# Kernel optimization log

Hardware: AMD Instinct MI355X
Metric: run time of the kernel (lower is better)

The kernel has to match this reference:

```python
import jax, jax.numpy as jnp
import numpy as np

B, T, H, W, C = 4, 16, 56, 56, 256
NH = 8
CS = (2, 7, 7)   # cuboid_size
SS = (1, 3, 3)   # shift_size


def _reorder(x):
    # (B,T,H,W,C) -> (B, num_cuboids, cuboid_volume, C), strategy 'lll'
    b = x.shape[0]
    bt, bh, bw = CS
    x = x.reshape(b, T // bt, bt, H // bh, bh, W // bw, bw, C)
    x = x.transpose(0, 1, 3, 5, 2, 4, 6, 7)
    return x.reshape(b, (T // bt) * (H // bh) * (W // bw), bt * bh * bw, C)


def _reorder_rev(x):
    b = x.shape[0]
    bt, bh, bw = CS
    x = x.reshape(b, T // bt, H // bh, W // bw, bt, bh, bw, C)
    x = x.transpose(0, 1, 4, 2, 5, 3, 6, 7)
    return x.reshape(b, T, H, W, C)


def _attn_mask():
    # shift-window mask, computed statically with numpy (no padding needed:
    # T,H,W divide CS exactly, so data_mask is all-ones)
    m = np.zeros((T, H, W))
    cnt = 0
    for t in (slice(-CS[0]), slice(-CS[0], -SS[0]), slice(-SS[0], None)):
        for h in (slice(-CS[1]), slice(-CS[1], -SS[1]), slice(-SS[1], None)):
            for w in (slice(-CS[2]), slice(-CS[2], -SS[2]), slice(-SS[2], None)):
                m[t, h, w] = cnt
                cnt += 1
    bt, bh, bw = CS
    m = m.reshape(T // bt, bt, H // bh, bh, W // bw, bw)
    m = m.transpose(0, 2, 4, 1, 3, 5).reshape(-1, bt * bh * bw)
    return jnp.asarray(m[:, None, :] == m[:, :, None])  # (num_cuboids, vol, vol)


def setup_inputs() -> dict:
    key = jax.random.key(0)
    k1, k2, k3 = jax.random.split(key, 3)
    return {
        "x": jax.random.normal(k1, (B, T, H, W, C), dtype=jnp.float32),
        "gamma": jnp.ones((C,), jnp.float32),
        "beta": jnp.zeros((C,), jnp.float32),
        "w_qkv": jax.random.normal(k2, (3 * C, C), jnp.float32) * 0.02,
        "w_proj": jax.random.normal(k3, (C, C), jnp.float32) * 0.02,
        "b_proj": jnp.zeros((C,), jnp.float32),
    }


def reference(x, gamma, beta, w_qkv, w_proj, b_proj):
    hd = C // NH
    scale = hd ** -0.5
    # pre-norm (LayerNorm, eps=1e-5, biased variance as in torch)
    mu = x.mean(-1, keepdims=True)
    var = x.var(-1, keepdims=True)
    xn = (x - mu) * jax.lax.rsqrt(var + 1e-5) * gamma + beta
    # shift then cuboid reorder
    xs = jnp.roll(xn, shift=(-SS[0], -SS[1], -SS[2]), axis=(1, 2, 3))
    r = _reorder(xs)                       # (B, nc, vol, C)
    nc, vol = r.shape[1], r.shape[2]
    qkv = jnp.einsum('bnvc,dc->bnvd', r, w_qkv).reshape(B, nc, vol, 3, NH, hd)
    qkv = qkv.transpose(3, 0, 4, 1, 2, 5)  # (3, B, NH, nc, vol, hd)
    q, k, v = qkv[0], qkv[1], qkv[2]
    mask = _attn_mask()                    # (nc, vol, vol) bool
    score = jnp.einsum('bhnic,bhnjc->bhnij', q * scale, k)
    score = jnp.where(mask, score, jnp.float32(-1e18))
    attn = jax.nn.softmax(score, axis=-1) * mask  # masked_softmax
    out = jnp.einsum('bhnij,bhnjc->bhnic', attn, v)
    out = out.transpose(0, 2, 3, 1, 4).reshape(B, nc, vol, C)
    out = jnp.einsum('bnvc,dc->bnvd', out, w_proj) + b_proj  # final proj
    y = _reorder_rev(out)
    y = jnp.roll(y, shift=(SS[0], SS[1], SS[2]), axis=(1, 2, 3))
    return y
```

## Files before the change

kernel.cpp:

```cpp
#include <hip/hip_runtime.h>
#include <hip/hip_bf16.h>

#define NC_  512
#define VOL_ 98

typedef __attribute__((ext_vector_type(8))) short bf16x8;
typedef __attribute__((ext_vector_type(4))) float f32x4;
typedef __attribute__((ext_vector_type(16))) float f32x16;
typedef unsigned int u32;
typedef unsigned short u16;

#define MFMA16(a,b,c) __builtin_amdgcn_mfma_f32_16x16x32_bf16((a),(b),(c),0,0,0)
#define MFMA32(a,b,c) __builtin_amdgcn_mfma_f32_32x32x16_bf16((a),(b),(c),0,0,0)

#define SWZ(r)   ((unsigned)(((r) & 7) << 4))
#define SWZ5(r)  ((unsigned)(((r) & 31) << 4))
#define SWZV(d)  ((unsigned)(((d) & 15) << 4))

__device__ __forceinline__ u16 f2bf(float f) {
    u32 u = __float_as_uint(f);
    u32 r = (u + 0x7fffu + ((u >> 16) & 1u)) >> 16;
    return (u16)r;
}
__device__ __forceinline__ u32 cvt_pk(float lo, float hi) {
    u32 r;
    asm("v_cvt_pk_bf16_f32 %0, %1, %2" : "=v"(r) : "v"(lo), "v"(hi));
    return r;
}

__global__ void k_conv(const float* __restrict__ wqkv, const float* __restrict__ wproj,
                       u16* __restrict__ o)
{
    int i = blockIdx.x * 256 + threadIdx.x;
    if (i < 196608) {
        float v = wqkv[i];
        if (i < 65536) v *= 0.17677669529663687f;
        o[i] = f2bf(v);
    } else if (i < 262144) {
        o[i] = f2bf(wproj[i - 196608]);
    }
}

__global__ __launch_bounds__(512, 4)
void k_attn(const float* __restrict__ x, const float* __restrict__ gamma,
            const float* __restrict__ beta, const u16* __restrict__ wbf,
            u16* __restrict__ ao)
{
    __shared__ __align__(16) u16 rn[VOL_ * 256];
    __shared__ __align__(16) u16 Qs[112 * 32];
    __shared__ __align__(16) u16 Ks[112 * 32];
    __shared__ __align__(16) u16 Vt[32 * 128];
    __shared__ u32 rowbase[112];
    __shared__ unsigned char labs[128];

    const int rawb = blockIdx.x;
    const int bid = ((rawb & 7) << 8) | (rawb >> 3);
    const int b  = bid >> 9, n = bid & 511;
    const int ti = n >> 6, hi = (n >> 3) & 7, wi = n & 7;
    const int tid = threadIdx.x;
    const int lane = tid & 63, wv = tid >> 6;
    const int c15 = lane & 15, g  = lane >> 4;
    const int c31 = lane & 31, g2 = lane >> 5;

    if (tid < 128) {
        int i = tid;
        int vt = (i >= 49) ? 1 : 0;
        int r  = i - vt * 49;
        int vh = r / 7, vw = r - vh * 7;
        int t = ti * 2 + vt, h = hi * 7 + vh, w = wi * 7 + vw;
        if (i < 112) {
            int ts = (t + 1) & 15;
            int hs = h + 3; if (hs >= 56) hs -= 56;
            int ws2 = w + 3; if (ws2 >= 56) ws2 -= 56;
            rowbase[i] = (i < VOL_) ? (u32)((((b * 16 + ts) * 56 + hs) * 56 + ws2) * 256) : 0u;
        }
        if (i < VOL_) {
            int tr = (t < 14) ? 0 : ((t < 15) ? 1 : 2);
            int hr = (h < 49) ? 0 : ((h < 53) ? 1 : 2);
            int wr = (w < 49) ? 0 : ((w < 53) ? 1 : 2);
            labs[i] = (unsigned char)(tr * 9 + hr * 3 + wr);
        } else {
            labs[i] = (unsigned char)255;
        }
    }
    if (tid < 256) {
        int d = tid >> 3, kp = 112 + (tid & 7) * 2;
        unsigned a = (unsigned)(d * 256 + kp * 2) ^ SWZV(d);
        *(u32*)((char*)Vt + a) = 0u;
    }
    __syncthreads();

    const float4 gm = *(const float4*)(gamma + lane * 4);
    const float4 be = *(const float4*)(beta  + lane * 4);
    for (int i = wv; i < VOL_; i += 8) {
        const float* xp = x + (size_t)rowbase[i] + lane * 4;
        float4 xv = *(const float4*)xp;
        float s  = xv.x + xv.y + xv.z + xv.w;
        float s2 = xv.x * xv.x + xv.y * xv.y + xv.z * xv.z + xv.w * xv.w;
        #pragma unroll
        for (int o = 1; o < 64; o <<= 1) { s += __shfl_xor(s, o); s2 += __shfl_xor(s2, o); }
        float mu  = s  * (1.0f / 256.0f);
        float var = s2 * (1.0f / 256.0f) - mu * mu;
        float rs  = rsqrtf(var + 1e-5f);
        unsigned a = ((unsigned)(i * 512 + lane * 8)) ^ SWZ5(i);
        uint2 pk2;
        pk2.x = cvt_pk((xv.x - mu) * rs * gm.x + be.x, (xv.y - mu) * rs * gm.y + be.y);
        pk2.y = cvt_pk((xv.z - mu) * rs * gm.z + be.z, (xv.w - mu) * rs * gm.w + be.w);
        *(uint2*)((char*)rn + a) = pk2;
    }

    u32 lab4[7];
    #pragma unroll
    for (int c = 0; c < 7; ++c) lab4[c] = *(const u32*)&labs[c * 16 + g * 4];

    for (int hh = 0; hh < 8; ++hh) {
        __syncthreads();

        for (int u = wv; u < 12; u += 8) {
            int proj = u >> 2, mt = u & 3;
            int arow = mt * 32 + c31; if (arow > 111) arow = 111;
            const u16* wb = wbf + (size_t)(proj * 256 + hh * 32 + c31) * 256 + g2 * 8;
            f32x16 acc = {0,0,0,0,0,0,0,0,0,0,0,0,0,0,0,0};
            #pragma unroll
            for (int half = 0; half < 2; ++half) {
                bf16x8 Bf[8];
                #pragma unroll
                for (int kk = 0; kk < 8; ++kk)
                    Bf[kk] = *(const bf16x8*)(wb + (half * 8 + kk) * 16);
                #pragma unroll
                for (int kk = 0; kk < 8; ++kk) {
                    unsigned a = (unsigned)(arow * 512 + (half * 8 + kk) * 32 + g2 * 16) ^ SWZ5(arow);
                    bf16x8 A = *(const bf16x8*)((const char*)rn + a);
                    acc = MFMA32(A, Bf[kk], acc);
                }
            }
            if (proj == 2) {
                #pragma unroll
                for (int r = 0; r < 16; r += 2) {
                    int kpos = mt * 32 + (r & 3) + 8 * (r >> 2) + 4 * g2;
                    float v0 = (kpos < VOL_)     ? acc[r]     : 0.f;
                    float v1 = (kpos + 1 < VOL_) ? acc[r + 1] : 0.f;
                    unsigned a = (unsigned)(c31 * 256 + kpos * 2) ^ SWZV(c31);
                    *(u32*)((char*)Vt + a) = cvt_pk(v0, v1);
                }
            } else {
                char* dst = (char*)((proj == 0) ? Qs : Ks);
                #pragma unroll
                for (int r = 0; r < 16; ++r) {
                    int grow = mt * 32 + (r & 3) + 8 * (r >> 2) + 4 * g2;
                    if (grow < 112) {
                        unsigned a = (unsigned)(grow * 64 + c31 * 2) ^ SWZ(grow);
                        *(u16*)(dst + a) = f2bf(acc[r]);
                    }
                }
            }
        }
        __syncthreads();

        for (int mt = wv; mt < 7; mt += 8) {
            int qrow = mt * 16 + c15;
            int labr = labs[qrow];
            u32 labr4 = (u32)labr * 0x01010101u;
            unsigned qa = (unsigned)(qrow * 64 + g * 16) ^ SWZ(qrow);
            bf16x8 qB = *(const bf16x8*)((const char*)Qs + qa);

            f32x4 s[7];
            #pragma unroll
            for (int c = 0; c < 7; ++c) {
                int krow = c * 16 + c15;
                unsigned ka = (unsigned)(krow * 64 + g * 16) ^ SWZ(krow);
                bf16x8 kA = *(const bf16x8*)((const char*)Ks + ka);
                f32x4 z = {0.f, 0.f, 0.f, 0.f};
                s[c] = MFMA16(kA, qB, z);
            }
            float mx = -1e30f;
            #pragma unroll
            for (int c = 0; c < 7; ++c) {
                u32 xo = lab4[c] ^ labr4;
                #pragma unroll
                for (int i = 0; i < 4; ++i) {
                    bool ok = ((xo >> (8 * i)) & 255u) == 0u;
                    mx = fmaxf(mx, ok ? s[c][i] : -1e30f);
                }
            }
            mx = fmaxf(mx, __shfl_xor(mx, 16));
            mx = fmaxf(mx, __shfl_xor(mx, 32));
            float lsum = 0.f;
            #pragma unroll
            for (int c = 0; c < 7; ++c) {
                u32 xo = lab4[c] ^ labr4;
                #pragma unroll
                for (int i = 0; i < 4; ++i) {
                    bool ok = ((xo >> (8 * i)) & 255u) == 0u;
                    float e = ok ? __expf(s[c][i] - mx) : 0.f;
                    s[c][i] = e;
                    lsum += e;
                }
            }
            lsum += __shfl_xor(lsum, 16);
            lsum += __shfl_xor(lsum, 32);
            float inv = 1.0f / lsum;
            u32 pk[8][2];
            #pragma unroll
            for (int c = 0; c < 7; ++c) {
                pk[c][0] = cvt_pk(s[c][0] * inv, s[c][1] * inv);
                pk[c][1] = cvt_pk(s[c][2] * inv, s[c][3] * inv);
            }
            pk[7][0] = 0u; pk[7][1] = 0u;

            f32x4 O0 = {0.f, 0.f, 0.f, 0.f}, O1 = {0.f, 0.f, 0.f, 0.f};
            const int src0 = c15 + 32 * (g & 1);
            const bool csel = (g >> 1) != 0;
            #pragma unroll
            for (int f = 0; f < 4; ++f) {
                union { bf16x8 v; u32 w[4]; } pa;
                #pragma unroll
                for (int w = 0; w < 4; ++w) {
                    int src = src0 + 16 * (w >> 1);
                    u32 r0 = (u32)__shfl((int)pk[2 * f][w & 1], src);
                    u32 r1 = (u32)__shfl((int)pk[2 * f + 1][w & 1], src);
                    pa.w[w] = csel ? r1 : r0;
                }
                unsigned av0 = (unsigned)(c15 * 256 + f * 64 + g * 16) ^ SWZV(c15);
                unsigned av1 = (unsigned)((16 + c15) * 256 + f * 64 + g * 16) ^ SWZV(16 + c15);
                bf16x8 vB0 = *(const bf16x8*)((const char*)Vt + av0);
                bf16x8 vB1 = *(const bf16x8*)((const char*)Vt + av1);
                O0 = MFMA16(pa.v, vB0, O0);
                O1 = MFMA16(pa.v, vB1, O1);
            }
            #pragma unroll
            for (int i = 0; i < 4; ++i) {
                int grow = mt * 16 + g * 4 + i;
                if (grow < VOL_) {
                    size_t base = ((size_t)bid * VOL_ + grow) * 256 + hh * 32;
                    ao[base + c15]      = f2bf(O0[i]);
                    ao[base + 16 + c15] = f2bf(O1[i]);
                }
            }
        }
    }
}

__global__ __launch_bounds__(512, 4)
void k_proj(const u16* __restrict__ ao, const u16* __restrict__ wpbf,
            const float* __restrict__ bp, float* __restrict__ y)
{
    __shared__ __align__(16) u16 tile[VOL_ * 256];
    __shared__ u32 rowbase[112];
    const int rawb = blockIdx.x;
    const int bid = ((rawb & 7) << 8) | (rawb >> 3);
    const int b  = bid >> 9, n = bid & 511;
    const int ti = n >> 6, hi = (n >> 3) & 7, wi = n & 7;
    const int tid = threadIdx.x;
    const int c31 = (tid & 63) & 31, g2 = (tid & 63) >> 5;
    const int wv = tid >> 6;

    if (tid < 112) {
        int i = tid;
        int vt = (i >= 49) ? 1 : 0;
        int r  = i - vt * 49;
        int vh = r / 7, vw = r - vh * 7;
        int t = ti * 2 + vt, h = hi * 7 + vh, w = wi * 7 + vw;
        int ts = (t + 1) & 15;
        int hs = h + 3; if (hs >= 56) hs -= 56;
        int ws2 = w + 3; if (ws2 >= 56) ws2 -= 56;
        rowbase[i] = (i < VOL_) ? (u32)((((b * 16 + ts) * 56 + hs) * 56 + ws2) * 256) : 0u;
    }
    const uint4* src = (const uint4*)(ao + (size_t)bid * (VOL_ * 256));
    for (int cidx = tid; cidx < (VOL_ * 256) / 8; cidx += 512) {
        uint4 v = src[cidx];
        int row = cidx >> 5, blk = cidx & 31;
        unsigned a = (unsigned)((row << 9) + (blk << 4)) ^ SWZ5(row);
        *(uint4*)((char*)tile + a) = v;
    }
    __syncthreads();

    for (int u = wv; u < 32; u += 8) {
        int nt = u >> 2, mt = u & 3;
        int arow = mt * 32 + c31; if (arow > 97) arow = 97;
        const u16* wb = wpbf + (size_t)(nt * 32 + c31) * 256 + g2 * 8;
        f32x16 acc = {0,0,0,0,0,0,0,0,0,0,0,0,0,0,0,0};
        #pragma unroll
        for (int half = 0; half < 2; ++half) {
            bf16x8 Bf[8];
            #pragma unroll
            for (int kk = 0; kk < 8; ++kk)
                Bf[kk] = *(const bf16x8*)(wb + (half * 8 + kk) * 16);
            #pragma unroll
            for (int kk = 0; kk < 8; ++kk) {
                unsigned a = (unsigned)(arow * 512 + (half * 8 + kk) * 32 + g2 * 16) ^ SWZ5(arow);
                bf16x8 A = *(const bf16x8*)((const char*)tile + a);
                acc = MFMA32(A, Bf[kk], acc);
            }
        }
        float bias = bp[nt * 32 + c31];
        #pragma unroll
        for (int r = 0; r < 16; ++r) {
            int row = (r & 3) + 8 * (r >> 2) + 4 * g2 + mt * 32;
            if (row < VOL_) {
                y[(size_t)rowbase[row] + nt * 32 + c31] = acc[r] + bias;
            }
        }
    }
}

extern "C" void kernel_launch(void* const* d_in, const int* in_sizes, int n_in,
                              void* d_out, int out_size, void* d_ws, size_t ws_size,
                              hipStream_t stream) {
    const float* x     = (const float*)d_in[0];
    const float* gamma = (const float*)d_in[1];
    const float* beta  = (const float*)d_in[2];
    const float* wqkv  = (const float*)d_in[3];
    const float* wproj = (const float*)d_in[4];
    const float* bproj = (const float*)d_in[5];
    float* y = (float*)d_out;

    u16* wbf  = (u16*)d_ws;
    u16* wpbf = wbf + 196608;
    u16* ao   = wbf + 262144;

    k_conv<<<dim3(1024), dim3(256), 0, stream>>>(wqkv, wproj, wbf);
    k_attn<<<dim3(4 * NC_), dim3(512), 0, stream>>>(x, gamma, beta, wbf, ao);
    k_proj<<<dim3(4 * NC_), dim3(512), 0, stream>>>(ao, wpbf, bproj, y);
}
```

Baseline: 613.1 us.

## Move Q projection into per-wave attention tiles to balance K/V projection work

The K and V projections (8 units) now map one-to-one onto the 8 waves, replacing the 12-unit round-robin where 4 waves did double work. Each attention wave computes its own 16-row Q tile with 16x16 MFMAs just before the score computation, which removes the Q projection from the shared stage. This trades a less imbalanced barrier-separated phase for some redundant A-operand LDS reads and an extra lgkmcnt wait. It also guards the softmax against a zero row sum.

```diff
diff --git a/kernel.cpp b/kernel.cpp
--- a/kernel.cpp
+++ b/kernel.cpp
@@ -90,23 +90,25 @@
     }
     __syncthreads();
 
-    const float4 gm = *(const float4*)(gamma + lane * 4);
-    const float4 be = *(const float4*)(beta  + lane * 4);
-    for (int i = wv; i < VOL_; i += 8) {
-        const float* xp = x + (size_t)rowbase[i] + lane * 4;
-        float4 xv = *(const float4*)xp;
-        float s  = xv.x + xv.y + xv.z + xv.w;
-        float s2 = xv.x * xv.x + xv.y * xv.y + xv.z * xv.z + xv.w * xv.w;
-        #pragma unroll
-        for (int o = 1; o < 64; o <<= 1) { s += __shfl_xor(s, o); s2 += __shfl_xor(s2, o); }
-        float mu  = s  * (1.0f / 256.0f);
-        float var = s2 * (1.0f / 256.0f) - mu * mu;
-        float rs  = rsqrtf(var + 1e-5f);
-        unsigned a = ((unsigned)(i * 512 + lane * 8)) ^ SWZ5(i);
-        uint2 pk2;
-        pk2.x = cvt_pk((xv.x - mu) * rs * gm.x + be.x, (xv.y - mu) * rs * gm.y + be.y);
-        pk2.y = cvt_pk((xv.z - mu) * rs * gm.z + be.z, (xv.w - mu) * rs * gm.w + be.w);
-        *(uint2*)((char*)rn + a) = pk2;
+    {
+        const float4 gm = *(const float4*)(gamma + lane * 4);
+        const float4 be = *(const float4*)(beta  + lane * 4);
+        for (int i = wv; i < VOL_; i += 8) {
+            const float* xp = x + (size_t)rowbase[i] + lane * 4;
+            float4 xv = *(const float4*)xp;
+            float s  = xv.x + xv.y + xv.z + xv.w;
+            float s2 = xv.x * xv.x + xv.y * xv.y + xv.z * xv.z + xv.w * xv.w;
+            #pragma unroll
+            for (int o = 1; o < 64; o <<= 1) { s += __shfl_xor(s, o); s2 += __shfl_xor(s2, o); }
+            float mu  = s  * (1.0f / 256.0f);
+            float var = s2 * (1.0f / 256.0f) - mu * mu;
+            float rs  = rsqrtf(var + 1e-5f);
+            unsigned a = ((unsigned)(i * 512 + lane * 8)) ^ SWZ5(i);
+            uint2 pk2;
+            pk2.x = cvt_pk((xv.x - mu) * rs * gm.x + be.x, (xv.y - mu) * rs * gm.y + be.y);
+            pk2.y = cvt_pk((xv.z - mu) * rs * gm.z + be.z, (xv.w - mu) * rs * gm.w + be.w);
+            *(uint2*)((char*)rn + a) = pk2;
+        }
     }
 
     u32 lab4[7];
@@ -116,8 +118,9 @@
     for (int hh = 0; hh < 8; ++hh) {
         __syncthreads();
 
-        for (int u = wv; u < 12; u += 8) {
-            int proj = u >> 2, mt = u & 3;
+        {
+            const int proj = (wv >> 2) + 1;
+            const int mt = wv & 3;
             int arow = mt * 32 + c31; if (arow > 111) arow = 111;
             const u16* wb = wbf + (size_t)(proj * 256 + hh * 32 + c31) * 256 + g2 * 8;
             f32x16 acc = {0,0,0,0,0,0,0,0,0,0,0,0,0,0,0,0};
@@ -144,20 +147,45 @@
                     *(u32*)((char*)Vt + a) = cvt_pk(v0, v1);
                 }
             } else {
-                char* dst = (char*)((proj == 0) ? Qs : Ks);
                 #pragma unroll
                 for (int r = 0; r < 16; ++r) {
                     int grow = mt * 32 + (r & 3) + 8 * (r >> 2) + 4 * g2;
                     if (grow < 112) {
                         unsigned a = (unsigned)(grow * 64 + c31 * 2) ^ SWZ(grow);
-                        *(u16*)(dst + a) = f2bf(acc[r]);
+                        *(u16*)((char*)Ks + a) = f2bf(acc[r]);
                     }
                 }
             }
         }
         __syncthreads();
 
-        for (int mt = wv; mt < 7; mt += 8) {
+        if (wv < 7) {
+            const int mt = wv;
+            {
+                int jr = mt * 16 + c15; if (jr > 97) jr = 97;
+                #pragma unroll
+                for (int ct = 0; ct < 2; ++ct) {
+                    const u16* wq = wbf + (size_t)(hh * 32 + ct * 16 + c15) * 256 + g * 8;
+                    f32x4 acc = {0.f, 0.f, 0.f, 0.f};
+                    #pragma unroll
+                    for (int kk = 0; kk < 8; ++kk) {
+                        unsigned a = (unsigned)(jr * 512 + kk * 64 + g * 16) ^ SWZ5(jr);
+                        bf16x8 A = *(const bf16x8*)((const char*)rn + a);
+                        bf16x8 B = *(const bf16x8*)(wq + kk * 32);
+                        acc = MFMA16(A, B, acc);
+                    }
+                    int colb = ct * 16 + c15;
+                    #pragma unroll
+                    for (int i = 0; i < 4; ++i) {
+                        int grow = mt * 16 + g * 4 + i;
+                        unsigned a = (unsigned)(grow * 64 + colb * 2) ^ SWZ(grow);
+                        *(u16*)((char*)Qs + a) = f2bf(acc[i]);
+                    }
+                }
+                asm volatile("s_waitcnt lgkmcnt(0)" ::: "memory");
+                __builtin_amdgcn_sched_barrier(0);
+            }
+
             int qrow = mt * 16 + c15;
             int labr = labs[qrow];
             u32 labr4 = (u32)labr * 0x01010101u;
@@ -199,7 +227,7 @@
             }
             lsum += __shfl_xor(lsum, 16);
             lsum += __shfl_xor(lsum, 32);
-            float inv = 1.0f / lsum;
+            float inv = (lsum > 0.f) ? (1.0f / lsum) : 0.f;
             u32 pk[8][2];
             #pragma unroll
             for (int c = 0; c < 7; ++c) {
@@ -208,7 +236,7 @@
             }
             pk[7][0] = 0u; pk[7][1] = 0u;
 
-            f32x4 O0 = {0.f, 0.f, 0.f, 0.f}, O1 = {0.f, 0.f, 0.f, 0.f};
+            f32x4 O0 = {0.f,0.f,0.f,0.f}, O1 = {0.f,0.f,0.f,0.f};
             const int src0 = c15 + 32 * (g & 1);
             const bool csel = (g >> 1) != 0;
             #pragma unroll
```

New measurement: 703.4 us. +14.7%, slower.

## Overlap next-head Q projection with attention via double-buffered Q tile

Applied to the files above, without the earlier changes.

Double-buffers the Q shared-memory tile. While waves 0-6 run attention for head hh, wave 7 computes the Q projection for head hh+1, so each later head only projects K and V (8 units across the 8 waves) inside the synchronized phase. The 32x32 GEMM unit is moved into a helper that splits accumulation across two independent MFMA chains to shorten the dependency chain. This costs extra LDS for the second Q buffer, and the lone Q-producing wave may become the critical path each iteration.

```diff
diff --git a/kernel.cpp b/kernel.cpp
--- a/kernel.cpp
+++ b/kernel.cpp
@@ -26,6 +26,27 @@
     u32 r;
     asm("v_cvt_pk_bf16_f32 %0, %1, %2" : "=v"(r) : "v"(lo), "v"(hi));
     return r;
+}
+
+__device__ __forceinline__ f32x16 unit32(const char* ab, const u16* wb,
+                                         int arow, int aoff) {
+    f32x16 a0 = {0,0,0,0,0,0,0,0,0,0,0,0,0,0,0,0};
+    f32x16 a1 = {0,0,0,0,0,0,0,0,0,0,0,0,0,0,0,0};
+    #pragma unroll
+    for (int half = 0; half < 2; ++half) {
+        bf16x8 Bf[8];
+        #pragma unroll
+        for (int kk = 0; kk < 8; ++kk)
+            Bf[kk] = *(const bf16x8*)(wb + (half * 8 + kk) * 16);
+        #pragma unroll
+        for (int kk = 0; kk < 8; ++kk) {
+            unsigned a = (unsigned)(arow * 512 + (half * 8 + kk) * 32 + aoff) ^ SWZ5(arow);
+            bf16x8 A = *(const bf16x8*)(ab + a);
+            if (kk & 1) a1 = MFMA32(A, Bf[kk], a1);
+            else        a0 = MFMA32(A, Bf[kk], a0);
+        }
+    }
+    return a0 + a1;
 }
 
 __global__ void k_conv(const float* __restrict__ wqkv, const float* __restrict__ wproj,
@@ -47,7 +68,7 @@
             u16* __restrict__ ao)
 {
     __shared__ __align__(16) u16 rn[VOL_ * 256];
-    __shared__ __align__(16) u16 Qs[112 * 32];
+    __shared__ __align__(16) u16 Qs[2][112 * 32];
     __shared__ __align__(16) u16 Ks[112 * 32];
     __shared__ __align__(16) u16 Vt[32 * 128];
     __shared__ u32 rowbase[112];
@@ -90,50 +111,69 @@
     }
     __syncthreads();
 
-    const float4 gm = *(const float4*)(gamma + lane * 4);
-    const float4 be = *(const float4*)(beta  + lane * 4);
-    for (int i = wv; i < VOL_; i += 8) {
-        const float* xp = x + (size_t)rowbase[i] + lane * 4;
-        float4 xv = *(const float4*)xp;
-        float s  = xv.x + xv.y + xv.z + xv.w;
-        float s2 = xv.x * xv.x + xv.y * xv.y + xv.z * xv.z + xv.w * xv.w;
-        #pragma unroll
-        for (int o = 1; o < 64; o <<= 1) { s += __shfl_xor(s, o); s2 += __shfl_xor(s2, o); }
-        float mu  = s  * (1.0f / 256.0f);
-        float var = s2 * (1.0f / 256.0f) - mu * mu;
-        float rs  = rsqrtf(var + 1e-5f);
-        unsigned a = ((unsigned)(i * 512 + lane * 8)) ^ SWZ5(i);
-        uint2 pk2;
-        pk2.x = cvt_pk((xv.x - mu) * rs * gm.x + be.x, (xv.y - mu) * rs * gm.y + be.y);
-        pk2.y = cvt_pk((xv.z - mu) * rs * gm.z + be.z, (xv.w - mu) * rs * gm.w + be.w);
-        *(uint2*)((char*)rn + a) = pk2;
+    {
+        const float4 gm = *(const float4*)(gamma + lane * 4);
+        const float4 be = *(const float4*)(beta  + lane * 4);
+        for (int i = wv; i < VOL_; i += 8) {
+            const float* xp = x + (size_t)rowbase[i] + lane * 4;
+            float4 xv = *(const float4*)xp;
+            float s  = xv.x + xv.y + xv.z + xv.w;
+            float s2 = xv.x * xv.x + xv.y * xv.y + xv.z * xv.z + xv.w * xv.w;
+            #pragma unroll
+            for (int o = 1; o < 64; o <<= 1) { s += __shfl_xor(s, o); s2 += __shfl_xor(s2, o); }
+            float mu  = s  * (1.0f / 256.0f);
+            float var = s2 * (1.0f / 256.0f) - mu * mu;
+            float rs  = rsqrtf(var + 1e-5f);
+            unsigned a = ((unsigned)(i * 512 + lane * 8)) ^ SWZ5(i);
+            uint2 pk2;
+            pk2.x = cvt_pk((xv.x - mu) * rs * gm.x + be.x, (xv.y - mu) * rs * gm.y + be.y);
+            pk2.y = cvt_pk((xv.z - mu) * rs * gm.z + be.z, (xv.w - mu) * rs * gm.w + be.w);
+            *(uint2*)((char*)rn + a) = pk2;
+        }
     }
 
     u32 lab4[7];
     #pragma unroll
     for (int c = 0; c < 7; ++c) lab4[c] = *(const u32*)&labs[c * 16 + g * 4];
 
+    const int aoff = g2 * 16;
+
     for (int hh = 0; hh < 8; ++hh) {
         __syncthreads();
 
-        for (int u = wv; u < 12; u += 8) {
-            int proj = u >> 2, mt = u & 3;
+        if (hh == 0) {
+            for (int u = wv; u < 12; u += 8) {
+                int proj = u >> 2, mt = u & 3;
+                int arow = mt * 32 + c31; if (arow > 111) arow = 111;
+                const u16* wb = wbf + (size_t)(proj * 256 + hh * 32 + c31) * 256 + g2 * 8;
+                f32x16 acc = unit32((const char*)rn, wb, arow, aoff);
+                if (proj == 2) {
+                    #pragma unroll
+                    for (int r = 0; r < 16; r += 2) {
+                        int kpos = mt * 32 + (r & 3) + 8 * (r >> 2) + 4 * g2;
+                        float v0 = (kpos < VOL_)     ? acc[r]     : 0.f;
+                        float v1 = (kpos + 1 < VOL_) ? acc[r + 1] : 0.f;
+                        unsigned a = (unsigned)(c31 * 256 + kpos * 2) ^ SWZV(c31);
+                        *(u32*)((char*)Vt + a) = cvt_pk(v0, v1);
+                    }
+                } else {
+                    char* dst = (char*)((proj == 0) ? &Qs[0][0] : Ks);
+                    #pragma unroll
+                    for (int r = 0; r < 16; ++r) {
+                        int grow = mt * 32 + (r & 3) + 8 * (r >> 2) + 4 * g2;
+                        if (grow < 112) {
+                            unsigned a = (unsigned)(grow * 64 + c31 * 2) ^ SWZ(grow);
+                            *(u16*)(dst + a) = f2bf(acc[r]);
+                        }
+                    }
+                }
+            }
+        } else {
+            const int proj = (wv >> 2) + 1;
+            const int mt = wv & 3;
             int arow = mt * 32 + c31; if (arow > 111) arow = 111;
             const u16* wb = wbf + (size_t)(proj * 256 + hh * 32 + c31) * 256 + g2 * 8;
-            f32x16 acc = {0,0,0,0,0,0,0,0,0,0,0,0,0,0,0,0};
-            #pragma unroll
-            for (int half = 0; half < 2; ++half) {
-                bf16x8 Bf[8];
-                #pragma unroll
-                for (int kk = 0; kk < 8; ++kk)
-                    Bf[kk] = *(const bf16x8*)(wb + (half * 8 + kk) * 16);
-                #pragma unroll
-                for (int kk = 0; kk < 8; ++kk) {
-                    unsigned a = (unsigned)(arow * 512 + (half * 8 + kk) * 32 + g2 * 16) ^ SWZ5(arow);
-                    bf16x8 A = *(const bf16x8*)((const char*)rn + a);
-                    acc = MFMA32(A, Bf[kk], acc);
-                }
-            }
+            f32x16 acc = unit32((const char*)rn, wb, arow, aoff);
             if (proj == 2) {
                 #pragma unroll
                 for (int r = 0; r < 16; r += 2) {
@@ -144,7 +184,108 @@
                     *(u32*)((char*)Vt + a) = cvt_pk(v0, v1);
                 }
             } else {
-                char* dst = (char*)((proj == 0) ? Qs : Ks);
+                #pragma unroll
+                for (int r = 0; r < 16; ++r) {
+                    int grow = mt * 32 + (r & 3) + 8 * (r >> 2) + 4 * g2;
+                    if (grow < 112) {
+                        unsigned a = (unsigned)(grow * 64 + c31 * 2) ^ SWZ(grow);
+                        *(u16*)((char*)Ks + a) = f2bf(acc[r]);
+                    }
+                }
+            }
+        }
+        __syncthreads();
+
+        if (wv < 7) {
+            const int mt = wv;
+            const char* Qb = (const char*)&Qs[hh & 1][0];
+            int qrow = mt * 16 + c15;
+            int labr = labs[qrow];
+            u32 labr4 = (u32)labr * 0x01010101u;
+            unsigned qa = (unsigned)(qrow * 64 + g * 16) ^ SWZ(qrow);
+            bf16x8 qB = *(const bf16x8*)(Qb + qa);
+
+            f32x4 s[7];
+            #pragma unroll
+            for (int c = 0; c < 7; ++c) {
+                int krow = c * 16 + c15;
+                unsigned ka = (unsigned)(krow * 64 + g * 16) ^ SWZ(krow);
+                bf16x8 kA = *(const bf16x8*)((const char*)Ks + ka);
+                f32x4 z = {0.f, 0.f, 0.f, 0.f};
+                s[c] = MFMA16(kA, qB, z);
+            }
+            float mx = -1e30f;
+            #pragma unroll
+            for (int c = 0; c < 7; ++c) {
+                u32 xo = lab4[c] ^ labr4;
+                #pragma unroll
+                for (int i = 0; i < 4; ++i) {
+                    bool ok = ((xo >> (8 * i)) & 255u) == 0u;
+                    mx = fmaxf(mx, ok ? s[c][i] : -1e30f);
+                }
+            }
+            mx = fmaxf(mx, __shfl_xor(mx, 16));
+            mx = fmaxf(mx, __shfl_xor(mx, 32));
+            float lsum = 0.f;
+            #pragma unroll
+            for (int c = 0; c < 7; ++c) {
+                u32 xo = lab4[c] ^ labr4;
+                #pragma unroll
+                for (int i = 0; i < 4; ++i) {
+                    bool ok = ((xo >> (8 * i)) & 255u) == 0u;
+                    float e = ok ? __expf(s[c][i] - mx) : 0.f;
+                    s[c][i] = e;
+                    lsum += e;
+                }
+            }
+            lsum += __shfl_xor(lsum, 16);
+            lsum += __shfl_xor(lsum, 32);
+            float inv = (lsum > 0.f) ? (1.0f / lsum) : 0.f;
+            u32 pk[8][2];
+            #pragma unroll
+            for (int c = 0; c < 7; ++c) {
+                pk[c][0] = cvt_pk(s[c][0] * inv, s[c][1] * inv);
+                pk[c][1] = cvt_pk(s[c][2] * inv, s[c][3] * inv);
+            }
+            pk[7][0] = 0u; pk[7][1] = 0u;
+
+            f32x4 O0 = {0.f,0.f,0.f,0.f}, O1 = {0.f,0.f,0.f,0.f};
+            const int src0 = c15 + 32 * (g & 1);
+            const bool csel = (g >> 1) != 0;
+            #pragma unroll
+            for (int f = 0; f < 4; ++f) {
+                union { bf16x8 v; u32 w[4]; } pa;
+                #pragma unroll
+                for (int w = 0; w < 4; ++w) {
+                    int src = src0 + 16 * (w >> 1);
+                    u32 r0 = (u32)__shfl((int)pk[2 * f][w & 1], src);
+                    u32 r1 = (u32)__shfl((int)pk[2 * f + 1][w & 1], src);
+                    pa.w[w] = csel ? r1 : r0;
+                }
+                unsigned av0 = (unsigned)(c15 * 256 + f * 64 + g * 16) ^ SWZV(c15);
+                unsigned av1 = (unsigned)((16 + c15) * 256 + f * 64 + g * 16) ^ SWZV(16 + c15);
+                bf16x8 vB0 = *(const bf16x8*)((const char*)Vt + av0);
+                bf16x8 vB1 = *(const bf16x8*)((const char*)Vt + av1);
+                O0 = MFMA16(pa.v, vB0, O0);
+                O1 = MFMA16(pa.v, vB1, O1);
+            }
+            #pragma unroll
+            for (int i = 0; i < 4; ++i) {
+                int grow = mt * 16 + g * 4 + i;
+                if (grow < VOL_) {
+                    size_t base = ((size_t)bid * VOL_ + grow) * 256 + hh * 32;
+                    ao[base + c15]      = f2bf(O0[i]);
+                    ao[base + 16 + c15] = f2bf(O1[i]);
+                }
+            }
+        } else if (hh < 7) {
+            const int hn = hh + 1;
+            char* dst = (char*)&Qs[hn & 1][0];
+            const u16* wb = wbf + (size_t)(hn * 32 + c31) * 256 + g2 * 8;
+            #pragma unroll 1
+            for (int mt = 0; mt < 4; ++mt) {
+                int arow = mt * 32 + c31; if (arow > 111) arow = 111;
+                f32x16 acc = unit32((const char*)rn, wb, arow, aoff);
                 #pragma unroll
                 for (int r = 0; r < 16; ++r) {
                     int grow = mt * 32 + (r & 3) + 8 * (r >> 2) + 4 * g2;
@@ -152,89 +293,6 @@
                         unsigned a = (unsigned)(grow * 64 + c31 * 2) ^ SWZ(grow);
                         *(u16*)(dst + a) = f2bf(acc[r]);
                     }
-                }
-            }
-        }
-        __syncthreads();
-
-        for (int mt = wv; mt < 7; mt += 8) {
-            int qrow = mt * 16 + c15;
-            int labr = labs[qrow];
-            u32 labr4 = (u32)labr * 0x01010101u;
-            unsigned qa = (unsigned)(qrow * 64 + g * 16) ^ SWZ(qrow);
-            bf16x8 qB = *(const bf16x8*)((const char*)Qs + qa);
-
-            f32x4 s[7];
-            #pragma unroll
-            for (int c = 0; c < 7; ++c) {
-                int krow = c * 16 + c15;
-                unsigned ka = (unsigned)(krow * 64 + g * 16) ^ SWZ(krow);
-                bf16x8 kA = *(const bf16x8*)((const char*)Ks + ka);
-                f32x4 z = {0.f, 0.f, 0.f, 0.f};
-                s[c] = MFMA16(kA, qB, z);
-            }
-            float mx = -1e30f;
-            #pragma unroll
-            for (int c = 0; c < 7; ++c) {
-                u32 xo = lab4[c] ^ labr4;
-                #pragma unroll
-                for (int i = 0; i < 4; ++i) {
-                    bool ok = ((xo >> (8 * i)) & 255u) == 0u;
-                    mx = fmaxf(mx, ok ? s[c][i] : -1e30f);
-                }
-            }
-            mx = fmaxf(mx, __shfl_xor(mx, 16));
-            mx = fmaxf(mx, __shfl_xor(mx, 32));
-            float lsum = 0.f;
-            #pragma unroll
-            for (int c = 0; c < 7; ++c) {
-                u32 xo = lab4[c] ^ labr4;
-                #pragma unroll
-                for (int i = 0; i < 4; ++i) {
-                    bool ok = ((xo >> (8 * i)) & 255u) == 0u;
-                    float e = ok ? __expf(s[c][i] - mx) : 0.f;
-                    s[c][i] = e;
-                    lsum += e;
-                }
-            }
-            lsum += __shfl_xor(lsum, 16);
-            lsum += __shfl_xor(lsum, 32);
-            float inv = 1.0f / lsum;
-            u32 pk[8][2];
-            #pragma unroll
-            for (int c = 0; c < 7; ++c) {
-                pk[c][0] = cvt_pk(s[c][0] * inv, s[c][1] * inv);
-                pk[c][1] = cvt_pk(s[c][2] * inv, s[c][3] * inv);
-            }
-            pk[7][0] = 0u; pk[7][1] = 0u;
-
-            f32x4 O0 = {0.f, 0.f, 0.f, 0.f}, O1 = {0.f, 0.f, 0.f, 0.f};
-            const int src0 = c15 + 32 * (g & 1);
-            const bool csel = (g >> 1) != 0;
-            #pragma unroll
-            for (int f = 0; f < 4; ++f) {
-                union { bf16x8 v; u32 w[4]; } pa;
-                #pragma unroll
-                for (int w = 0; w < 4; ++w) {
-                    int src = src0 + 16 * (w >> 1);
-                    u32 r0 = (u32)__shfl((int)pk[2 * f][w & 1], src);
-                    u32 r1 = (u32)__shfl((int)pk[2 * f + 1][w & 1], src);
-                    pa.w[w] = csel ? r1 : r0;
-                }
-                unsigned av0 = (unsigned)(c15 * 256 + f * 64 + g * 16) ^ SWZV(c15);
-                unsigned av1 = (unsigned)((16 + c15) * 256 + f * 64 + g * 16) ^ SWZV(16 + c15);
-                bf16x8 vB0 = *(const bf16x8*)((const char*)Vt + av0);
-                bf16x8 vB1 = *(const bf16x8*)((const char*)Vt + av1);
-                O0 = MFMA16(pa.v, vB0, O0);
-                O1 = MFMA16(pa.v, vB1, O1);
-            }
-            #pragma unroll
-            for (int i = 0; i < 4; ++i) {
-                int grow = mt * 16 + g * 4 + i;
-                if (grow < VOL_) {
-                    size_t base = ((size_t)bid * VOL_ + grow) * 256 + hh * 32;
-                    ao[base + c15]      = f2bf(O0[i]);
-                    ao[base + 16 + c15] = f2bf(O1[i]);
                 }
             }
         }
@@ -275,24 +333,12 @@
     }
     __syncthreads();
 
+    const int aoff = g2 * 16;
     for (int u = wv; u < 32; u += 8) {
         int nt = u >> 2, mt = u & 3;
         int arow = mt * 32 + c31; if (arow > 97) arow = 97;
         const u16* wb = wpbf + (size_t)(nt * 32 + c31) * 256 + g2 * 8;
-        f32x16 acc = {0,0,0,0,0,0,0,0,0,0,0,0,0,0,0,0};
-        #pragma unroll
-        for (int half = 0; half < 2; ++half) {
-            bf16x8 Bf[8];
-            #pragma unroll
-            for (int kk = 0; kk < 8; ++kk)
-                Bf[kk] = *(const bf16x8*)(wb + (half * 8 + kk) * 16);
-            #pragma unroll
-            for (int kk = 0; kk < 8; ++kk) {
-                unsigned a = (unsigned)(arow * 512 + (half * 8 + kk) * 32 + g2 * 16) ^ SWZ5(arow);
-                bf16x8 A = *(const bf16x8*)((const char*)tile + a);
-                acc = MFMA32(A, Bf[kk], acc);
-            }
-        }
+        f32x16 acc = unit32((const char*)tile, wb, arow, aoff);
         float bias = bp[nt * 32 + c31];
         #pragma unroll
         for (int r = 0; r < 16; ++r) {
```

Measured after the change: 963.0 us. 57.1% more time.
